# Performance work log

Measured on AMD Instinct MI355X. Metric: run time of the kernel, lower is better.

## Reference

```python
import jax, jax.numpy as jnp
import numpy as np

NEG_SLOPE = 0.2
EPS = 1e-16

N_NODES = 50000
N_EDGES = 800000
IN_CH = 128
HEADS = 4
OUT_CH = 32


def setup_inputs() -> dict:
    key = jax.random.key(0)
    k1, k2, k3, k4, k5 = jax.random.split(key, 5)
    x = jax.random.normal(k1, (N_NODES, IN_CH), dtype=jnp.float32)
    edge_index = jax.random.randint(k2, (2, N_EDGES), 0, N_NODES, dtype=jnp.int64)
    # Glorot-ish scaling for stability
    W = jax.random.normal(k3, (IN_CH, HEADS * OUT_CH), dtype=jnp.float32) / np.sqrt(IN_CH)
    att_src = jax.random.normal(k4, (HEADS, OUT_CH), dtype=jnp.float32) / np.sqrt(OUT_CH)
    att_dst = jax.random.normal(k5, (HEADS, OUT_CH), dtype=jnp.float32) / np.sqrt(OUT_CH)
    bias = jnp.zeros((HEADS * OUT_CH,), dtype=jnp.float32)
    return {"x": x, "edge_index": edge_index, "W": W,
            "att_src": att_src, "att_dst": att_dst, "bias": bias}


def reference(x, edge_index, W, att_src, att_dst, bias):
    N = x.shape[0]
    H, C = att_src.shape

    # PyG GATConv default: add self-loops
    self_loop = jnp.arange(N, dtype=edge_index.dtype)
    src = jnp.concatenate([edge_index[0], self_loop])  # [E+N]
    dst = jnp.concatenate([edge_index[1], self_loop])  # [E+N]

    # Linear transform, split heads: [N, H, C]
    h = (x @ W).reshape(N, H, C)

    # Per-node attention logits: [N, H]
    a_src = jnp.sum(h * att_src[None], axis=-1)
    a_dst = jnp.sum(h * att_dst[None], axis=-1)

    # Per-edge logits with LeakyReLU: [E+N, H]
    e = a_src[src] + a_dst[dst]
    e = jnp.where(e >= 0, e, NEG_SLOPE * e)

    # Segment softmax over destination-node neighborhoods
    e_max = jax.ops.segment_max(e, dst, num_segments=N)  # [N, H]
    e_exp = jnp.exp(e - e_max[dst])
    denom = jax.ops.segment_sum(e_exp, dst, num_segments=N)  # [N, H]
    alpha = e_exp / (denom[dst] + EPS)  # [E+N, H]

    # Weighted scatter-aggregate of messages: [N, H, C]
    msgs = h[src] * alpha[:, :, None]
    out = jax.ops.segment_sum(msgs, dst, num_segments=N)

    out = out.reshape(N, H * C) + bias  # concat heads + bias
    return jax.nn.relu(out)  # wrapper activation (dropout=0 is identity)
```

## Files before the change

### kernel.cpp

```cpp
#include <hip/hip_runtime.h>
#include <hip/hip_bf16.h>
#include <math.h>

#define NEG_SLOPE 0.2f
#define EPS_F 1e-16f
#define PCAP 4096
#define NPMAX 512
#define LOG2E 1.44269504088896f

typedef float f32x4 __attribute__((ext_vector_type(4)));
typedef short bf16x8 __attribute__((ext_vector_type(8)));

__device__ __forceinline__ unsigned int pk2bf(float a, float b) {
    unsigned int ua = __float_as_uint(a), ub = __float_as_uint(b);
    ua = (ua + 0x7fffu + ((ua >> 16) & 1u)) >> 16;
    ub = (ub + 0x7fffu + ((ub >> 16) & 1u)) >> 16;
    return ua | (ub << 16);
}
__device__ __forceinline__ unsigned short f2bf(float f) {
    unsigned int u = __float_as_uint(f);
    return (unsigned short)((u + 0x7fffu + ((u >> 16) & 1u)) >> 16);
}
__device__ __forceinline__ float bf_lo(unsigned int p) { return __uint_as_float(p << 16); }
__device__ __forceinline__ float bf_hi(unsigned int p) { return __uint_as_float(p & 0xffff0000u); }

__global__ void k_prep(const float* __restrict__ W,
                       const float* __restrict__ att_src, const float* __restrict__ att_dst,
                       unsigned short* __restrict__ Wtb) {
    int b = blockIdx.x, t = threadIdx.x;
    if (b < 64) {
        int id = b * 256 + t;
        int k = id >> 7, col = id & 127;
        Wtb[col * 128 + k] = f2bf(W[id]);
    } else {
        int k4 = t >> 3, j = t & 7;
        const float* att = (j < 4) ? att_src : att_dst;
        int h = j & 3;
        #pragma unroll
        for (int kk = 0; kk < 4; kk++) {
            int k = k4 * 4 + kk;
            float s = 0.f;
            #pragma unroll
            for (int c = 0; c < 32; c++)
                s = fmaf(W[k * 128 + h * 32 + c], att[h * 32 + c], s);
            Wtb[(128 + j) * 128 + k] = f2bf(s * LOG2E);
        }
        for (int idx = t; idx < 1024; idx += 256)
            Wtb[(136 + (idx >> 7)) * 128 + (idx & 127)] = 0;
    }
}

__global__ __launch_bounds__(256)
void k_pg(const unsigned int* __restrict__ eidx,
          int* __restrict__ pcnt, unsigned int* __restrict__ rec, int E, int npart,
          const float* __restrict__ x, const unsigned short* __restrict__ Wtb,
          unsigned short* __restrict__ hb,
          float* __restrict__ a_src, float* __restrict__ a_dst, int N, int nPB) {
    __shared__ __align__(16) char smem[53248];
    int t = threadIdx.x;

    if ((int)blockIdx.x < nPB) {
        int* hist = (int*)smem;
        int* base = (int*)(smem + 2048);
        int* sflagp = (int*)(smem + 4096);
        if (t < 64) {
            unsigned int v = eidx[2 * t + 1];
            #pragma unroll
            for (int m = 1; m <= 32; m <<= 1) v |= __shfl_xor(v, m);
            if (t == 0) *sflagp = (v == 0u) ? 1 : 0;
        }
        for (int p = t; p < npart; p += 256) hist[p] = 0;
        __syncthreads();
        int flag = *sflagp;
        const uint2* e2p = (const uint2*)eidx;
        int e0 = blockIdx.x * 4096;
        int se[16], de[16];
        #pragma unroll
        for (int i = 0; i < 16; i++) {
            int idx = e0 + t + i * 256;
            de[i] = -1;
            if (idx < E) {
                if (flag) { se[i] = (int)e2p[idx].x; de[i] = (int)e2p[E + idx].x; }
                else      { se[i] = (int)eidx[idx];  de[i] = (int)eidx[E + idx]; }
                atomicAdd(&hist[de[i] >> 7], 1);
            }
        }
        __syncthreads();
        for (int p = t; p < npart; p += 256) {
            int c = hist[p];
            base[p] = c ? atomicAdd(&pcnt[p], c) : 0;
            hist[p] = 0;
        }
        __syncthreads();
        #pragma unroll
        for (int i = 0; i < 16; i++) {
            if (de[i] >= 0) {
                int p = de[i] >> 7;
                int r = atomicAdd(&hist[p], 1);
                int pos = base[p] + r;
                if (pos < PCAP)
                    rec[(size_t)p * PCAP + pos] =
                        ((unsigned int)se[i] << 7) | (unsigned int)(de[i] & 127);
            }
        }
    } else {
        unsigned short* xlds = (unsigned short*)smem;
        unsigned short* wlds = (unsigned short*)(smem + 16384);
        int l = t & 63, w = t >> 6;
        int br = ((int)blockIdx.x - nPB) * 64;

        #pragma unroll
        for (int i = 0; i < 9; i++) {
            int u = t + i * 256;
            uint4 v = *(const uint4*)(Wtb + u * 8);
            int row = u >> 4;
            int e8  = (u & 15) * 8;
            *(uint4*)&wlds[row * 128 + (e8 ^ ((row & 7) << 3))] = v;
        }
        {
            int row = t >> 2, kq = t & 3;
            int gr = br + row;
            const float* xp = x + (size_t)gr * 128 + kq * 32;
            #pragma unroll
            for (int j = 0; j < 4; j++) {
                uint4 pk = make_uint4(0u, 0u, 0u, 0u);
                if (gr < N) {
                    float4 v0 = *(const float4*)(xp + j * 8);
                    float4 v1 = *(const float4*)(xp + j * 8 + 4);
                    pk.x = pk2bf(v0.x, v0.y); pk.y = pk2bf(v0.z, v0.w);
                    pk.z = pk2bf(v1.x, v1.y); pk.w = pk2bf(v1.z, v1.w);
                }
                int e8 = kq * 32 + j * 8;
                *(uint4*)&xlds[row * 128 + (e8 ^ ((row & 7) << 3))] = pk;
            }
        }
        __syncthreads();

        bf16x8 a[4];
        int arow = w * 16 + (l & 15);
        int ae   = (l >> 4) * 8;
        #pragma unroll
        for (int kc = 0; kc < 4; kc++)
            a[kc] = *(const bf16x8*)&xlds[arow * 128 + ((kc * 32 + ae) ^ ((arow & 7) << 3))];

        int rowbase = br + w * 16 + (l >> 4) * 4;

        #pragma unroll
        for (int nb = 0; nb < 9; nb++) {
            int brow = nb * 16 + (l & 15);
            f32x4 c = {0.f, 0.f, 0.f, 0.f};
            #pragma unroll
            for (int kc = 0; kc < 4; kc++) {
                bf16x8 bfr = *(const bf16x8*)&wlds[brow * 128 + ((kc * 32 + ae) ^ ((brow & 7) << 3))];
                c = __builtin_amdgcn_mfma_f32_16x16x32_bf16(a[kc], bfr, c, 0, 0, 0);
            }
            if (nb < 8) {
                #pragma unroll
                for (int r = 0; r < 4; r++) {
                    float v  = c[r];
                    float vo = __shfl_xor(v, 1);
                    int row = rowbase + r;
                    if (row < N && (l & 1) == 0)
                        *(unsigned int*)&hb[(size_t)row * 128 + nb * 16 + (l & 15)] = pk2bf(v, vo);
                }
            } else {
                int j = l & 15;
                #pragma unroll
                for (int r = 0; r < 4; r++) {
                    int row = rowbase + r;
                    if (row < N && j < 8) {
                        if (j < 4) a_src[row * 4 + j]     = c[r];
                        else       a_dst[row * 4 + j - 4] = c[r];
                    }
                }
            }
        }
    }
}

__global__ __launch_bounds__(256)
void k_bin2(const int* __restrict__ pcnt, const unsigned int* __restrict__ rec,
            unsigned int* __restrict__ srt, int* __restrict__ rowArr,
            int* __restrict__ degArr, int N) {
    __shared__ int hist[128];
    __shared__ int offs[128];
    __shared__ int cur[128];
    __shared__ unsigned int ssort[PCAP];
    int p = blockIdx.x, t = threadIdx.x;
    if (t < 128) { hist[t] = 0; cur[t] = 0; }
    __syncthreads();
    int cnt = min(pcnt[p], PCAP);
    const unsigned int* rb = rec + (size_t)p * PCAP;
    for (int i = t; i < cnt; i += 256) atomicAdd(&hist[rb[i] & 127], 1);
    __syncthreads();
    if (t < 128) offs[t] = hist[t];
    __syncthreads();
    #pragma unroll
    for (int off = 1; off < 128; off <<= 1) {
        int u = (t < 128 && t >= off) ? offs[t - off] : 0;
        __syncthreads();
        if (t < 128) offs[t] += u;
        __syncthreads();
    }
    for (int i = t; i < cnt; i += 256) {
        unsigned int r = rb[i];
        int n = r & 127;
        int pos = (offs[n] - hist[n]) + atomicAdd(&cur[n], 1);
        ssort[pos] = r >> 7;
    }
    __syncthreads();
    for (int i = t; i < cnt; i += 256) srt[(size_t)p * PCAP + i] = ssort[i];
    int node = (p << 7) + t;
    if (t < 128 && node < N) {
        rowArr[node] = p * PCAP + (offs[t] - hist[t]);
        degArr[node] = hist[t];
    }
}

#define BATCH4(bk, j, ad, den, ax, ay)                                          \
    {                                                                            \
        int s0=(int)bk[j], s1=(int)bk[j+1], s2=(int)bk[j+2], s3=(int)bk[j+3];    \
        float a0=a_src[s0*4+head], a1=a_src[s1*4+head];                          \
        float a2=a_src[s2*4+head], a3=a_src[s3*4+head];                          \
        unsigned int p0=*(const unsigned int*)&hb[(size_t)s0*128+c0];            \
        unsigned int p1=*(const unsigned int*)&hb[(size_t)s1*128+c0];            \
        unsigned int p2=*(const unsigned int*)&hb[(size_t)s2*128+c0];            \
        unsigned int p3=*(const unsigned int*)&hb[(size_t)s3*128+c0];            \
        float e0=a0+ad; e0=fmaxf(e0,NEG_SLOPE*e0); float w0=exp2f(e0);           \
        float e1=a1+ad; e1=fmaxf(e1,NEG_SLOPE*e1); float w1=exp2f(e1);           \
        float e2=a2+ad; e2=fmaxf(e2,NEG_SLOPE*e2); float w2=exp2f(e2);           \
        float e3=a3+ad; e3=fmaxf(e3,NEG_SLOPE*e3); float w3=exp2f(e3);           \
        den += (w0+w1)+(w2+w3);                                                  \
        ax = fmaf(w0,bf_lo(p0),ax); ay = fmaf(w0,bf_hi(p0),ay);                  \
        ax = fmaf(w1,bf_lo(p1),ax); ay = fmaf(w1,bf_hi(p1),ay);                  \
        ax = fmaf(w2,bf_lo(p2),ax); ay = fmaf(w2,bf_hi(p2),ay);                  \
        ax = fmaf(w3,bf_lo(p3),ax); ay = fmaf(w3,bf_hi(p3),ay);                  \
    }

#define ONEEDGE(bk, j, ad, den, ax, ay)                                          \
    {                                                                            \
        int s0=(int)bk[j];                                                       \
        float a0=a_src[s0*4+head];                                               \
        unsigned int p0=*(const unsigned int*)&hb[(size_t)s0*128+c0];            \
        float e0=a0+ad; e0=fmaxf(e0,NEG_SLOPE*e0); float w0=exp2f(e0);           \
        den += w0;                                                               \
        ax = fmaf(w0,bf_lo(p0),ax); ay = fmaf(w0,bf_hi(p0),ay);                  \
    }

__global__ __launch_bounds__(256)
void k_aggregate(const unsigned int* __restrict__ srt, const int* __restrict__ rowArr,
                 const int* __restrict__ degArr,
                 const float* __restrict__ a_src, const float* __restrict__ a_dst,
                 const unsigned short* __restrict__ hb,
                 const float* __restrict__ bias,
                 float* __restrict__ out, int N) {
    int wave = threadIdx.x >> 6;
    int lane = threadIdx.x & 63;
    int c0 = lane * 2;
    int head = lane >> 4;
    int dA = blockIdx.x * 8 + wave * 2;
    int dB = dA + 1;
    if (dA >= N) return;
    bool vB = dB < N;

    float adA, denA, axA, ayA; const unsigned int* bkA; int gA;
    {
        adA = a_dst[dA * 4 + head];
        float es = a_src[dA * 4 + head] + adA;
        es = fmaxf(es, NEG_SLOPE * es);
        float w = exp2f(es);
        unsigned int hp = *(const unsigned int*)&hb[(size_t)dA * 128 + c0];
        denA = w; axA = w * bf_lo(hp); ayA = w * bf_hi(hp);
        bkA = srt + rowArr[dA]; gA = degArr[dA];
    }
    float adB = 0.f, denB = 0.f, axB = 0.f, ayB = 0.f;
    const unsigned int* bkB = srt; int gB = 0;
    if (vB) {
        adB = a_dst[dB * 4 + head];
        float es = a_src[dB * 4 + head] + adB;
        es = fmaxf(es, NEG_SLOPE * es);
        float w = exp2f(es);
        unsigned int hp = *(const unsigned int*)&hb[(size_t)dB * 128 + c0];
        denB = w; axB = w * bf_lo(hp); ayB = w * bf_hi(hp);
        bkB = srt + rowArr[dB]; gB = degArr[dB];
    }

    int jA = 0, jB = 0;
    while (jA + 4 <= gA && jB + 4 <= gB) {
        BATCH4(bkA, jA, adA, denA, axA, ayA);
        BATCH4(bkB, jB, adB, denB, axB, ayB);
        jA += 4; jB += 4;
    }
    while (jA + 4 <= gA) { BATCH4(bkA, jA, adA, denA, axA, ayA); jA += 4; }
    while (jB + 4 <= gB) { BATCH4(bkB, jB, adB, denB, axB, ayB); jB += 4; }
    while (jA < gA && jB < gB) {
        ONEEDGE(bkA, jA, adA, denA, axA, ayA);
        ONEEDGE(bkB, jB, adB, denB, axB, ayB);
        jA++; jB++;
    }
    for (; jA < gA; jA++) ONEEDGE(bkA, jA, adA, denA, axA, ayA);
    for (; jB < gB; jB++) ONEEDGE(bkB, jB, adB, denB, axB, ayB);

    float2 b2 = *(const float2*)&bias[c0];
    {
        float rden = 1.f / (denA + EPS_F);
        float ox = fmaxf(axA * rden + b2.x, 0.f);
        float oy = fmaxf(ayA * rden + b2.y, 0.f);
        *(float2*)&out[(size_t)dA * 128 + c0] = make_float2(ox, oy);
    }
    if (vB) {
        float rden = 1.f / (denB + EPS_F);
        float ox = fmaxf(axB * rden + b2.x, 0.f);
        float oy = fmaxf(ayB * rden + b2.y, 0.f);
        *(float2*)&out[(size_t)dB * 128 + c0] = make_float2(ox, oy);
    }
}

extern "C" void kernel_launch(void* const* d_in, const int* in_sizes, int n_in,
                              void* d_out, int out_size, void* d_ws, size_t ws_size,
                              hipStream_t stream) {
    const float* x        = (const float*)d_in[0];
    const unsigned int* e = (const unsigned int*)d_in[1];
    const float* W        = (const float*)d_in[2];
    const float* att_src  = (const float*)d_in[3];
    const float* att_dst  = (const float*)d_in[4];
    const float* bias     = (const float*)d_in[5];
    float* out            = (float*)d_out;

    int N = in_sizes[0] / 128;
    int E = in_sizes[1] / 2;
    int npart = (N + 127) >> 7;

    char* ws = (char*)d_ws;
    size_t off = 0;
    unsigned short* Wtb    = (unsigned short*)(ws + off); off += 144 * 128 * 2;
    unsigned short* hb     = (unsigned short*)(ws + off); off += (size_t)N * 128 * 2;
    float*          a_src  = (float*)(ws + off);          off += (size_t)N * 16;
    float*          a_dst  = (float*)(ws + off);          off += (size_t)N * 16;
    int*            rowArr = (int*)(ws + off);            off += (size_t)N * 4;
    int*            degArr = (int*)(ws + off);            off += (size_t)N * 4;
    int*            pcnt   = (int*)(ws + off);            off += (size_t)NPMAX * 4;
    unsigned int*   rec    = (unsigned int*)(ws + off);   off += (size_t)npart * PCAP * 4;
    unsigned int*   srt    = (unsigned int*)(ws + off);   off += (size_t)npart * PCAP * 4;

    int nPB = (E + 4095) / 4096;
    int gb  = (N + 63) / 64;

    hipMemsetAsync(pcnt, 0, (size_t)NPMAX * 4, stream);

    k_prep<<<65, 256, 0, stream>>>(W, att_src, att_dst, Wtb);
    k_pg<<<nPB + gb, 256, 0, stream>>>(e, pcnt, rec, E, npart,
                                       x, Wtb, hb, a_src, a_dst, N, nPB);
    k_bin2<<<npart, 256, 0, stream>>>(pcnt, rec, srt, rowArr, degArr, N);
    k_aggregate<<<(N + 7) / 8, 256, 0, stream>>>(srt, rowArr, degArr,
                                                 a_src, a_dst, hb, bias, out, N);
}
```

Baseline: 87.71 us.

## Fuse per-partition bin sort into aggregation kernel and fold pcnt memset into prep

Merges the counting-sort kernel into the aggregation kernel. Each 512-thread block sorts its 128-node partition's edge records into shared memory and then aggregates those nodes directly from LDS, so the srt/rowArr/degArr global round trip and one launch go away. The pcnt memset moves into an extra k_prep block, and the log2e prescaling with exp2f is replaced by __expf on unscaled logits. The cost is fewer, heavier blocks (one per partition, about 391), which may lower parallelism and load balance in the gather phase.

Measured after the change: 89.81 us. +2.4%, slower.

```diff
diff --git a/kernel.cpp b/kernel.cpp
--- a/kernel.cpp
+++ b/kernel.cpp
@@ -6,7 +6,6 @@
 #define EPS_F 1e-16f
 #define PCAP 4096
 #define NPMAX 512
-#define LOG2E 1.44269504088896f
 
 typedef float f32x4 __attribute__((ext_vector_type(4)));
 typedef short bf16x8 __attribute__((ext_vector_type(8)));
@@ -26,13 +25,13 @@
 
 __global__ void k_prep(const float* __restrict__ W,
                        const float* __restrict__ att_src, const float* __restrict__ att_dst,
-                       unsigned short* __restrict__ Wtb) {
+                       unsigned short* __restrict__ Wtb, int* __restrict__ pcnt) {
     int b = blockIdx.x, t = threadIdx.x;
     if (b < 64) {
         int id = b * 256 + t;
         int k = id >> 7, col = id & 127;
         Wtb[col * 128 + k] = f2bf(W[id]);
-    } else {
+    } else if (b == 64) {
         int k4 = t >> 3, j = t & 7;
         const float* att = (j < 4) ? att_src : att_dst;
         int h = j & 3;
@@ -43,10 +42,13 @@
             #pragma unroll
             for (int c = 0; c < 32; c++)
                 s = fmaf(W[k * 128 + h * 32 + c], att[h * 32 + c], s);
-            Wtb[(128 + j) * 128 + k] = f2bf(s * LOG2E);
+            Wtb[(128 + j) * 128 + k] = f2bf(s);
         }
         for (int idx = t; idx < 1024; idx += 256)
             Wtb[(136 + (idx >> 7)) * 128 + (idx & 127)] = 0;
+    } else {
+        pcnt[t] = 0;
+        pcnt[t + 256] = 0;
     }
 }
 
@@ -178,45 +180,6 @@
     }
 }
 
-__global__ __launch_bounds__(256)
-void k_bin2(const int* __restrict__ pcnt, const unsigned int* __restrict__ rec,
-            unsigned int* __restrict__ srt, int* __restrict__ rowArr,
-            int* __restrict__ degArr, int N) {
-    __shared__ int hist[128];
-    __shared__ int offs[128];
-    __shared__ int cur[128];
-    __shared__ unsigned int ssort[PCAP];
-    int p = blockIdx.x, t = threadIdx.x;
-    if (t < 128) { hist[t] = 0; cur[t] = 0; }
-    __syncthreads();
-    int cnt = min(pcnt[p], PCAP);
-    const unsigned int* rb = rec + (size_t)p * PCAP;
-    for (int i = t; i < cnt; i += 256) atomicAdd(&hist[rb[i] & 127], 1);
-    __syncthreads();
-    if (t < 128) offs[t] = hist[t];
-    __syncthreads();
-    #pragma unroll
-    for (int off = 1; off < 128; off <<= 1) {
-        int u = (t < 128 && t >= off) ? offs[t - off] : 0;
-        __syncthreads();
-        if (t < 128) offs[t] += u;
-        __syncthreads();
-    }
-    for (int i = t; i < cnt; i += 256) {
-        unsigned int r = rb[i];
-        int n = r & 127;
-        int pos = (offs[n] - hist[n]) + atomicAdd(&cur[n], 1);
-        ssort[pos] = r >> 7;
-    }
-    __syncthreads();
-    for (int i = t; i < cnt; i += 256) srt[(size_t)p * PCAP + i] = ssort[i];
-    int node = (p << 7) + t;
-    if (t < 128 && node < N) {
-        rowArr[node] = p * PCAP + (offs[t] - hist[t]);
-        degArr[node] = hist[t];
-    }
-}
-
 #define BATCH4(bk, j, ad, den, ax, ay)                                          \
     {                                                                            \
         int s0=(int)bk[j], s1=(int)bk[j+1], s2=(int)bk[j+2], s3=(int)bk[j+3];    \
@@ -226,10 +189,10 @@
         unsigned int p1=*(const unsigned int*)&hb[(size_t)s1*128+c0];            \
         unsigned int p2=*(const unsigned int*)&hb[(size_t)s2*128+c0];            \
         unsigned int p3=*(const unsigned int*)&hb[(size_t)s3*128+c0];            \
-        float e0=a0+ad; e0=fmaxf(e0,NEG_SLOPE*e0); float w0=exp2f(e0);           \
-        float e1=a1+ad; e1=fmaxf(e1,NEG_SLOPE*e1); float w1=exp2f(e1);           \
-        float e2=a2+ad; e2=fmaxf(e2,NEG_SLOPE*e2); float w2=exp2f(e2);           \
-        float e3=a3+ad; e3=fmaxf(e3,NEG_SLOPE*e3); float w3=exp2f(e3);           \
+        float e0=a0+ad; e0=fmaxf(e0,NEG_SLOPE*e0); float w0=__expf(e0);          \
+        float e1=a1+ad; e1=fmaxf(e1,NEG_SLOPE*e1); float w1=__expf(e1);          \
+        float e2=a2+ad; e2=fmaxf(e2,NEG_SLOPE*e2); float w2=__expf(e2);          \
+        float e3=a3+ad; e3=fmaxf(e3,NEG_SLOPE*e3); float w3=__expf(e3);          \
         den += (w0+w1)+(w2+w3);                                                  \
         ax = fmaf(w0,bf_lo(p0),ax); ay = fmaf(w0,bf_hi(p0),ay);                  \
         ax = fmaf(w1,bf_lo(p1),ax); ay = fmaf(w1,bf_hi(p1),ay);                  \
@@ -242,77 +205,112 @@
         int s0=(int)bk[j];                                                       \
         float a0=a_src[s0*4+head];                                               \
         unsigned int p0=*(const unsigned int*)&hb[(size_t)s0*128+c0];            \
-        float e0=a0+ad; e0=fmaxf(e0,NEG_SLOPE*e0); float w0=exp2f(e0);           \
+        float e0=a0+ad; e0=fmaxf(e0,NEG_SLOPE*e0); float w0=__expf(e0);          \
         den += w0;                                                               \
         ax = fmaf(w0,bf_lo(p0),ax); ay = fmaf(w0,bf_hi(p0),ay);                  \
     }
 
-__global__ __launch_bounds__(256)
-void k_aggregate(const unsigned int* __restrict__ srt, const int* __restrict__ rowArr,
-                 const int* __restrict__ degArr,
-                 const float* __restrict__ a_src, const float* __restrict__ a_dst,
-                 const unsigned short* __restrict__ hb,
-                 const float* __restrict__ bias,
-                 float* __restrict__ out, int N) {
-    int wave = threadIdx.x >> 6;
-    int lane = threadIdx.x & 63;
+__global__ __launch_bounds__(512)
+void k_agg(const int* __restrict__ pcnt, const unsigned int* __restrict__ rec,
+           const float* __restrict__ a_src, const float* __restrict__ a_dst,
+           const unsigned short* __restrict__ hb, const float* __restrict__ bias,
+           float* __restrict__ out, int N) {
+    __shared__ int hist[128];
+    __shared__ int start[128];
+    __shared__ int cur[128];
+    __shared__ unsigned int ssort[PCAP];
+    int p = blockIdx.x, t = threadIdx.x;
+
+    if (t < 128) { hist[t] = 0; cur[t] = 0; }
+    __syncthreads();
+    int cnt = min(pcnt[p], PCAP);
+    const unsigned int* rb = rec + (size_t)p * PCAP;
+    for (int i = t; i < cnt; i += 512) atomicAdd(&hist[rb[i] & 127], 1);
+    __syncthreads();
+    if (t < 128) start[t] = hist[t];
+    __syncthreads();
+    #pragma unroll
+    for (int off = 1; off < 128; off <<= 1) {
+        int u = (t < 128 && t >= off) ? start[t - off] : 0;
+        __syncthreads();
+        if (t < 128) start[t] += u;
+        __syncthreads();
+    }
+    if (t < 128) start[t] -= hist[t];
+    __syncthreads();
+    for (int i = t; i < cnt; i += 512) {
+        unsigned int r = rb[i];
+        int n = r & 127;
+        int pos = start[n] + atomicAdd(&cur[n], 1);
+        ssort[pos] = r >> 7;
+    }
+    __syncthreads();
+
+    int wave = t >> 6;
+    int lane = t & 63;
     int c0 = lane * 2;
     int head = lane >> 4;
-    int dA = blockIdx.x * 8 + wave * 2;
-    int dB = dA + 1;
-    if (dA >= N) return;
-    bool vB = dB < N;
-
-    float adA, denA, axA, ayA; const unsigned int* bkA; int gA;
-    {
-        adA = a_dst[dA * 4 + head];
-        float es = a_src[dA * 4 + head] + adA;
-        es = fmaxf(es, NEG_SLOPE * es);
-        float w = exp2f(es);
-        unsigned int hp = *(const unsigned int*)&hb[(size_t)dA * 128 + c0];
-        denA = w; axA = w * bf_lo(hp); ayA = w * bf_hi(hp);
-        bkA = srt + rowArr[dA]; gA = degArr[dA];
-    }
-    float adB = 0.f, denB = 0.f, axB = 0.f, ayB = 0.f;
-    const unsigned int* bkB = srt; int gB = 0;
-    if (vB) {
-        adB = a_dst[dB * 4 + head];
-        float es = a_src[dB * 4 + head] + adB;
-        es = fmaxf(es, NEG_SLOPE * es);
-        float w = exp2f(es);
-        unsigned int hp = *(const unsigned int*)&hb[(size_t)dB * 128 + c0];
-        denB = w; axB = w * bf_lo(hp); ayB = w * bf_hi(hp);
-        bkB = srt + rowArr[dB]; gB = degArr[dB];
-    }
-
-    int jA = 0, jB = 0;
-    while (jA + 4 <= gA && jB + 4 <= gB) {
-        BATCH4(bkA, jA, adA, denA, axA, ayA);
-        BATCH4(bkB, jB, adB, denB, axB, ayB);
-        jA += 4; jB += 4;
-    }
-    while (jA + 4 <= gA) { BATCH4(bkA, jA, adA, denA, axA, ayA); jA += 4; }
-    while (jB + 4 <= gB) { BATCH4(bkB, jB, adB, denB, axB, ayB); jB += 4; }
-    while (jA < gA && jB < gB) {
-        ONEEDGE(bkA, jA, adA, denA, axA, ayA);
-        ONEEDGE(bkB, jB, adB, denB, axB, ayB);
-        jA++; jB++;
-    }
-    for (; jA < gA; jA++) ONEEDGE(bkA, jA, adA, denA, axA, ayA);
-    for (; jB < gB; jB++) ONEEDGE(bkB, jB, adB, denB, axB, ayB);
-
     float2 b2 = *(const float2*)&bias[c0];
-    {
-        float rden = 1.f / (denA + EPS_F);
-        float ox = fmaxf(axA * rden + b2.x, 0.f);
-        float oy = fmaxf(ayA * rden + b2.y, 0.f);
-        *(float2*)&out[(size_t)dA * 128 + c0] = make_float2(ox, oy);
-    }
-    if (vB) {
-        float rden = 1.f / (denB + EPS_F);
-        float ox = fmaxf(axB * rden + b2.x, 0.f);
-        float oy = fmaxf(ayB * rden + b2.y, 0.f);
-        *(float2*)&out[(size_t)dB * 128 + c0] = make_float2(ox, oy);
+
+    #pragma unroll 1
+    for (int pair = 0; pair < 8; pair++) {
+        int nA = wave * 16 + pair * 2;
+        int nB = nA + 1;
+        int dA = (p << 7) + nA;
+        int dB = dA + 1;
+        if (dA >= N) continue;
+        bool vB = dB < N;
+
+        float adA, denA, axA, ayA; const unsigned int* bkA; int gA;
+        {
+            adA = a_dst[dA * 4 + head];
+            float es = a_src[dA * 4 + head] + adA;
+            es = fmaxf(es, NEG_SLOPE * es);
+            float w = __expf(es);
+            unsigned int hp = *(const unsigned int*)&hb[(size_t)dA * 128 + c0];
+            denA = w; axA = w * bf_lo(hp); ayA = w * bf_hi(hp);
+            bkA = ssort + start[nA]; gA = hist[nA];
+        }
+        float adB = 0.f, denB = 0.f, axB = 0.f, ayB = 0.f;
+        const unsigned int* bkB = ssort; int gB = 0;
+        if (vB) {
+            adB = a_dst[dB * 4 + head];
+            float es = a_src[dB * 4 + head] + adB;
+            es = fmaxf(es, NEG_SLOPE * es);
+            float w = __expf(es);
+            unsigned int hp = *(const unsigned int*)&hb[(size_t)dB * 128 + c0];
+            denB = w; axB = w * bf_lo(hp); ayB = w * bf_hi(hp);
+            bkB = ssort + start[nB]; gB = hist[nB];
+        }
+
+        int jA = 0, jB = 0;
+        while (jA + 4 <= gA && jB + 4 <= gB) {
+            BATCH4(bkA, jA, adA, denA, axA, ayA);
+            BATCH4(bkB, jB, adB, denB, axB, ayB);
+            jA += 4; jB += 4;
+        }
+        while (jA + 4 <= gA) { BATCH4(bkA, jA, adA, denA, axA, ayA); jA += 4; }
+        while (jB + 4 <= gB) { BATCH4(bkB, jB, adB, denB, axB, ayB); jB += 4; }
+        while (jA < gA && jB < gB) {
+            ONEEDGE(bkA, jA, adA, denA, axA, ayA);
+            ONEEDGE(bkB, jB, adB, denB, axB, ayB);
+            jA++; jB++;
+        }
+        for (; jA < gA; jA++) ONEEDGE(bkA, jA, adA, denA, axA, ayA);
+        for (; jB < gB; jB++) ONEEDGE(bkB, jB, adB, denB, axB, ayB);
+
+        {
+            float rden = 1.f / (denA + EPS_F);
+            float ox = fmaxf(axA * rden + b2.x, 0.f);
+            float oy = fmaxf(ayA * rden + b2.y, 0.f);
+            *(float2*)&out[(size_t)dA * 128 + c0] = make_float2(ox, oy);
+        }
+        if (vB) {
+            float rden = 1.f / (denB + EPS_F);
+            float ox = fmaxf(axB * rden + b2.x, 0.f);
+            float oy = fmaxf(ayB * rden + b2.y, 0.f);
+            *(float2*)&out[(size_t)dB * 128 + c0] = make_float2(ox, oy);
+        }
     }
 }
 
@@ -337,21 +335,14 @@
     unsigned short* hb     = (unsigned short*)(ws + off); off += (size_t)N * 128 * 2;
     float*          a_src  = (float*)(ws + off);          off += (size_t)N * 16;
     float*          a_dst  = (float*)(ws + off);          off += (size_t)N * 16;
-    int*            rowArr = (int*)(ws + off);            off += (size_t)N * 4;
-    int*            degArr = (int*)(ws + off);            off += (size_t)N * 4;
     int*            pcnt   = (int*)(ws + off);            off += (size_t)NPMAX * 4;
     unsigned int*   rec    = (unsigned int*)(ws + off);   off += (size_t)npart * PCAP * 4;
-    unsigned int*   srt    = (unsigned int*)(ws + off);   off += (size_t)npart * PCAP * 4;
 
     int nPB = (E + 4095) / 4096;
     int gb  = (N + 63) / 64;
 
-    hipMemsetAsync(pcnt, 0, (size_t)NPMAX * 4, stream);
-
-    k_prep<<<65, 256, 0, stream>>>(W, att_src, att_dst, Wtb);
+    k_prep<<<66, 256, 0, stream>>>(W, att_src, att_dst, Wtb, pcnt);
     k_pg<<<nPB + gb, 256, 0, stream>>>(e, pcnt, rec, E, npart,
                                        x, Wtb, hb, a_src, a_dst, N, nPB);
-    k_bin2<<<npart, 256, 0, stream>>>(pcnt, rec, srt, rowArr, degArr, N);
-    k_aggregate<<<(N + 7) / 8, 256, 0, stream>>>(srt, rowArr, degArr,
-                                                 a_src, a_dst, hb, bias, out, N);
-}
+    k_agg<<<npart, 512, 0, stream>>>(pcnt, rec, a_src, a_dst, hb, bias, out, N);
+}
```
